# Kernel optimization log

Measured on AMD Instinct MI355X. Metric: run time of the kernel, lower is better.

The kernel has to match this reference:

```python
import jax, jax.numpy as jnp
import numpy as np

B = 16384
C = 2048  # in_channel
OUT = 2   # out_channel


def setup_inputs() -> dict:
    key = jax.random.key(0)
    k1, k2, k3, k4, k5, k6, k7 = jax.random.split(key, 7)
    scale = 1.0 / np.sqrt(3 * C)  # torch Linear default init range
    return {
        "s_f": jax.random.normal(k1, (B, C), dtype=jnp.float32),
        "g_f": jax.random.normal(k2, (B, C), dtype=jnp.float32),
        "v_f": jax.random.normal(k3, (B, C), dtype=jnp.float32),
        "W_aff": jax.random.uniform(k4, (3 * C, 3), dtype=jnp.float32, minval=-scale, maxval=scale),
        "b_aff": jax.random.uniform(k5, (3,), dtype=jnp.float32, minval=-scale, maxval=scale),
        "W_cls": jax.random.uniform(k6, (3 * C, OUT), dtype=jnp.float32, minval=-scale, maxval=scale),
        "b_cls": jax.random.uniform(k7, (OUT,), dtype=jnp.float32, minval=-scale, maxval=scale),
    }


def reference(s_f, g_f, v_f, W_aff, b_aff, W_cls, b_cls):
    # Attention gating over the three modalities.
    x_att = jnp.concatenate([s_f, g_f, v_f], axis=1)          # [B, 3C]
    att = jax.nn.softmax(x_att @ W_aff + b_aff, axis=1)       # [B, 3]
    # diag(att[:, i]) @ f  ==  per-row scalar scaling (broadcast multiply).
    s = att[:, 0:1] * s_f
    g = att[:, 1:2] * g_f
    v = att[:, 2:3] * v_f
    x = jnp.concatenate([s, g, v], axis=1)                    # [B, 3C]
    return jax.nn.softmax(x @ W_cls + b_cls, axis=1)          # [B, OUT]
```

## Files before the change

### kernel.cpp

```cpp
#include <hip/hip_runtime.h>

#define B_ROWS 16384
#define C_DIM  2048
#define BLK    512
#define CPT    4
#define RPB    32
#define RB     4
#define NITER  (RPB / RB)
#define GROUP  8
#define NWAVE  (BLK / 64)
#define NACC   5

#define DPP_ADD(v, ctrl, rmask) \
  v += __int_as_float(__builtin_amdgcn_update_dpp(0, __float_as_int(v), (ctrl), (rmask), 0xf, false))

__device__ __forceinline__ float wave_sum16(float v) {
  DPP_ADD(v, 0x111, 0xf);
  DPP_ADD(v, 0x112, 0xf);
  DPP_ADD(v, 0x114, 0xf);
  DPP_ADD(v, 0x118, 0xf);
  return v;
}

__global__ __launch_bounds__(BLK)
void maff_partial(const float* __restrict__ s_f,
                  const float* __restrict__ g_f,
                  const float* __restrict__ v_f,
                  const float* __restrict__ W_aff,
                  const float* __restrict__ W_cls,
                  float* __restrict__ ws)
{
  const int t    = threadIdx.x;
  const int lane = t & 63;
  const int wave = t >> 6;
  const int grp  = lane >> 4;
  const int m    = blockIdx.y;
  const int row0 = blockIdx.x * RPB;
  const int c0   = t * CPT;

  const float* f = (m == 0) ? s_f : (m == 1) ? g_f : v_f;

  float wa[CPT][3];
  float wc[CPT][2];
  {
    const float4* pa = (const float4*)(W_aff + ((size_t)m * C_DIM + c0) * 3);
    float4 a0 = pa[0], a1 = pa[1], a2 = pa[2];
    wa[0][0]=a0.x; wa[0][1]=a0.y; wa[0][2]=a0.z;
    wa[1][0]=a0.w; wa[1][1]=a1.x; wa[1][2]=a1.y;
    wa[2][0]=a1.z; wa[2][1]=a1.w; wa[2][2]=a2.x;
    wa[3][0]=a2.y; wa[3][1]=a2.z; wa[3][2]=a2.w;
    const float4* pc = (const float4*)(W_cls + ((size_t)m * C_DIM + c0) * 2);
    float4 q0 = pc[0], q1 = pc[1];
    wc[0][0]=q0.x; wc[0][1]=q0.y; wc[1][0]=q0.z; wc[1][1]=q0.w;
    wc[2][0]=q1.x; wc[2][1]=q1.y; wc[3][0]=q1.z; wc[3][1]=q1.w;
  }

  __shared__ float red[2][GROUP][NWAVE][4][NACC];

  const float* base = f + (size_t)row0 * C_DIM + c0;

  float4 cur[RB];
#pragma unroll
  for (int k = 0; k < RB; ++k)
    cur[k] = *(const float4*)(base + (size_t)k * C_DIM);

  for (int it = 0; it < NITER; ++it) {
    const int nit = (it + 1 < NITER) ? (it + 1) : it;
    float4 nxt[RB];
#pragma unroll
    for (int k = 0; k < RB; ++k)
      nxt[k] = *(const float4*)(base + (size_t)(nit * RB + k) * C_DIM);

    float acc[RB][NACC];
#pragma unroll
    for (int k = 0; k < RB; ++k) {
      float x[CPT] = {cur[k].x, cur[k].y, cur[k].z, cur[k].w};
      float p0 = 0.f, p1 = 0.f, p2 = 0.f, q0 = 0.f, q1 = 0.f;
#pragma unroll
      for (int i = 0; i < CPT; ++i) {
        p0 = fmaf(x[i], wa[i][0], p0);
        p1 = fmaf(x[i], wa[i][1], p1);
        p2 = fmaf(x[i], wa[i][2], p2);
        q0 = fmaf(x[i], wc[i][0], q0);
        q1 = fmaf(x[i], wc[i][1], q1);
      }
      acc[k][0] = p0; acc[k][1] = p1; acc[k][2] = p2;
      acc[k][3] = q0; acc[k][4] = q1;
    }

#pragma unroll
    for (int k = 0; k < RB; ++k)
#pragma unroll
      for (int j = 0; j < NACC; ++j)
        acc[k][j] = wave_sum16(acc[k][j]);

    const int g  = it >> 1;
    const int gb = g & 1;
#pragma unroll
    for (int k = 0; k < RB; ++k) {
      const int r  = it * RB + k;
      const int gs = r & (GROUP - 1);
      if ((lane & 15) == 15) {
        float* d = &red[gb][gs][wave][grp][0];
        d[0] = acc[k][0]; d[1] = acc[k][1]; d[2] = acc[k][2];
        d[3] = acc[k][3]; d[4] = acc[k][4];
      }
    }

    if (it & 1) {
      __syncthreads();
      if (t < GROUP) {
        float s[NACC] = {0.f, 0.f, 0.f, 0.f, 0.f};
        const float* z = &red[gb][t][0][0][0];
#pragma unroll
        for (int w = 0; w < NWAVE * 4; ++w)
#pragma unroll
          for (int j = 0; j < NACC; ++j)
            s[j] += z[w * NACC + j];
        const int row = row0 + g * GROUP + t;
#pragma unroll
        for (int j = 0; j < NACC; ++j)
          ws[(m * NACC + j) * B_ROWS + row] = s[j];
      }
    }

#pragma unroll
    for (int k = 0; k < RB; ++k) cur[k] = nxt[k];
  }
}

__global__ __launch_bounds__(256)
void maff_epilogue(const float* __restrict__ ws,
                   const float* __restrict__ b_aff,
                   const float* __restrict__ b_cls,
                   float* __restrict__ out)
{
  const int row = blockIdx.x * 256 + threadIdx.x;

  float P[3][NACC];
#pragma unroll
  for (int m = 0; m < 3; ++m)
#pragma unroll
    for (int j = 0; j < NACC; ++j)
      P[m][j] = ws[(m * NACC + j) * B_ROWS + row];

  float A0 = P[0][0] + P[1][0] + P[2][0] + b_aff[0];
  float A1 = P[0][1] + P[1][1] + P[2][1] + b_aff[1];
  float A2 = P[0][2] + P[1][2] + P[2][2] + b_aff[2];

  float mx = fmaxf(A0, fmaxf(A1, A2));
  float e0 = __expf(A0 - mx), e1 = __expf(A1 - mx), e2 = __expf(A2 - mx);
  float inv = 1.0f / (e0 + e1 + e2);
  float t0 = e0 * inv, t1 = e1 * inv, t2 = e2 * inv;

  float L0 = t0 * P[0][3] + t1 * P[1][3] + t2 * P[2][3] + b_cls[0];
  float L1 = t0 * P[0][4] + t1 * P[1][4] + t2 * P[2][4] + b_cls[1];
  float mm = fmaxf(L0, L1);
  float x0 = __expf(L0 - mm), x1 = __expf(L1 - mm);
  float is = 1.0f / (x0 + x1);

  *(float2*)(out + (size_t)row * 2) = make_float2(x0 * is, x1 * is);
}

extern "C" void kernel_launch(void* const* d_in, const int* in_sizes, int n_in,
                              void* d_out, int out_size, void* d_ws, size_t ws_size,
                              hipStream_t stream) {
  const float* s_f   = (const float*)d_in[0];
  const float* g_f   = (const float*)d_in[1];
  const float* v_f   = (const float*)d_in[2];
  const float* W_aff = (const float*)d_in[3];
  const float* b_aff = (const float*)d_in[4];
  const float* W_cls = (const float*)d_in[5];
  const float* b_cls = (const float*)d_in[6];
  float* out = (float*)d_out;
  float* ws  = (float*)d_ws;

  dim3 grid1(B_ROWS / RPB, 3);
  maff_partial<<<grid1, dim3(BLK), 0, stream>>>(s_f, g_f, v_f, W_aff, W_cls, ws);

  dim3 grid2(B_ROWS / 256);
  maff_epilogue<<<grid2, dim3(256), 0, stream>>>(ws, b_aff, b_cls, out);
}
```

Measured before the change: 362.0 us.

## Assign rows per wave with weights in LDS, eliminating block-level reductions

```diff
diff --git a/kernel.cpp b/kernel.cpp
--- a/kernel.cpp
+++ b/kernel.cpp
@@ -3,24 +3,14 @@
 #define B_ROWS 16384
 #define C_DIM  2048
 #define BLK    512
-#define CPT    4
-#define RPB    32
-#define RB     4
-#define NITER  (RPB / RB)
-#define GROUP  8
 #define NWAVE  (BLK / 64)
+#define RPW    4
+#define RPB    (NWAVE * RPW)
 #define NACC   5
+#define NCHUNK (C_DIM / 256)
 
 #define DPP_ADD(v, ctrl, rmask) \
   v += __int_as_float(__builtin_amdgcn_update_dpp(0, __float_as_int(v), (ctrl), (rmask), 0xf, false))
-
-__device__ __forceinline__ float wave_sum16(float v) {
-  DPP_ADD(v, 0x111, 0xf);
-  DPP_ADD(v, 0x112, 0xf);
-  DPP_ADD(v, 0x114, 0xf);
-  DPP_ADD(v, 0x118, 0xf);
-  return v;
-}
 
 __global__ __launch_bounds__(BLK)
 void maff_partial(const float* __restrict__ s_f,
@@ -33,99 +23,77 @@
   const int t    = threadIdx.x;
   const int lane = t & 63;
   const int wave = t >> 6;
-  const int grp  = lane >> 4;
   const int m    = blockIdx.y;
-  const int row0 = blockIdx.x * RPB;
-  const int c0   = t * CPT;
+  const int row0 = blockIdx.x * RPB + wave * RPW;
 
   const float* f = (m == 0) ? s_f : (m == 1) ? g_f : v_f;
 
-  float wa[CPT][3];
-  float wc[CPT][2];
+  __shared__ float4 W[NACC][BLK];
   {
-    const float4* pa = (const float4*)(W_aff + ((size_t)m * C_DIM + c0) * 3);
+    const float4* pa = (const float4*)(W_aff + ((size_t)m * C_DIM + t * 4) * 3);
     float4 a0 = pa[0], a1 = pa[1], a2 = pa[2];
-    wa[0][0]=a0.x; wa[0][1]=a0.y; wa[0][2]=a0.z;
-    wa[1][0]=a0.w; wa[1][1]=a1.x; wa[1][2]=a1.y;
-    wa[2][0]=a1.z; wa[2][1]=a1.w; wa[2][2]=a2.x;
-    wa[3][0]=a2.y; wa[3][1]=a2.z; wa[3][2]=a2.w;
-    const float4* pc = (const float4*)(W_cls + ((size_t)m * C_DIM + c0) * 2);
+    const float4* pc = (const float4*)(W_cls + ((size_t)m * C_DIM + t * 4) * 2);
     float4 q0 = pc[0], q1 = pc[1];
-    wc[0][0]=q0.x; wc[0][1]=q0.y; wc[1][0]=q0.z; wc[1][1]=q0.w;
-    wc[2][0]=q1.x; wc[2][1]=q1.y; wc[3][0]=q1.z; wc[3][1]=q1.w;
+    W[0][t] = make_float4(a0.x, a0.w, a1.z, a2.y);
+    W[1][t] = make_float4(a0.y, a1.x, a1.w, a2.z);
+    W[2][t] = make_float4(a0.z, a1.y, a2.x, a2.w);
+    W[3][t] = make_float4(q0.x, q0.z, q1.x, q1.z);
+    W[4][t] = make_float4(q0.y, q0.w, q1.y, q1.w);
+  }
+  __syncthreads();
+
+  const float4* wp = &W[0][lane];
+  const float*  fb = f + (size_t)row0 * C_DIM + lane * 4;
+
+  float acc[RPW][NACC];
+#pragma unroll
+  for (int r = 0; r < RPW; ++r)
+#pragma unroll
+    for (int j = 0; j < NACC; ++j)
+      acc[r][j] = 0.f;
+
+#pragma unroll
+  for (int ch = 0; ch < NCHUNK; ++ch) {
+    float4 x[RPW];
+#pragma unroll
+    for (int r = 0; r < RPW; ++r)
+      x[r] = *(const float4*)(fb + (size_t)r * C_DIM + ch * 256);
+
+    float4 wv[NACC];
+#pragma unroll
+    for (int j = 0; j < NACC; ++j)
+      wv[j] = wp[j * BLK + ch * 64];
+
+#pragma unroll
+    for (int r = 0; r < RPW; ++r)
+#pragma unroll
+      for (int j = 0; j < NACC; ++j)
+        acc[r][j] = fmaf(x[r].w, wv[j].w,
+                    fmaf(x[r].z, wv[j].z,
+                    fmaf(x[r].y, wv[j].y,
+                    fmaf(x[r].x, wv[j].x, acc[r][j]))));
   }
 
-  __shared__ float red[2][GROUP][NWAVE][4][NACC];
-
-  const float* base = f + (size_t)row0 * C_DIM + c0;
-
-  float4 cur[RB];
 #pragma unroll
-  for (int k = 0; k < RB; ++k)
-    cur[k] = *(const float4*)(base + (size_t)k * C_DIM);
-
-  for (int it = 0; it < NITER; ++it) {
-    const int nit = (it + 1 < NITER) ? (it + 1) : it;
-    float4 nxt[RB];
+  for (int r = 0; r < RPW; ++r)
 #pragma unroll
-    for (int k = 0; k < RB; ++k)
-      nxt[k] = *(const float4*)(base + (size_t)(nit * RB + k) * C_DIM);
-
-    float acc[RB][NACC];
-#pragma unroll
-    for (int k = 0; k < RB; ++k) {
-      float x[CPT] = {cur[k].x, cur[k].y, cur[k].z, cur[k].w};
-      float p0 = 0.f, p1 = 0.f, p2 = 0.f, q0 = 0.f, q1 = 0.f;
-#pragma unroll
-      for (int i = 0; i < CPT; ++i) {
-        p0 = fmaf(x[i], wa[i][0], p0);
-        p1 = fmaf(x[i], wa[i][1], p1);
-        p2 = fmaf(x[i], wa[i][2], p2);
-        q0 = fmaf(x[i], wc[i][0], q0);
-        q1 = fmaf(x[i], wc[i][1], q1);
-      }
-      acc[k][0] = p0; acc[k][1] = p1; acc[k][2] = p2;
-      acc[k][3] = q0; acc[k][4] = q1;
+    for (int j = 0; j < NACC; ++j) {
+      float v = acc[r][j];
+      DPP_ADD(v, 0x111, 0xf);
+      DPP_ADD(v, 0x112, 0xf);
+      DPP_ADD(v, 0x114, 0xf);
+      DPP_ADD(v, 0x118, 0xf);
+      DPP_ADD(v, 0x142, 0xa);
+      DPP_ADD(v, 0x143, 0xc);
+      acc[r][j] = v;
     }
 
+  if (lane == 63) {
 #pragma unroll
-    for (int k = 0; k < RB; ++k)
+    for (int r = 0; r < RPW; ++r)
 #pragma unroll
       for (int j = 0; j < NACC; ++j)
-        acc[k][j] = wave_sum16(acc[k][j]);
-
-    const int g  = it >> 1;
-    const int gb = g & 1;
-#pragma unroll
-    for (int k = 0; k < RB; ++k) {
-      const int r  = it * RB + k;
-      const int gs = r & (GROUP - 1);
-      if ((lane & 15) == 15) {
-        float* d = &red[gb][gs][wave][grp][0];
-        d[0] = acc[k][0]; d[1] = acc[k][1]; d[2] = acc[k][2];
-        d[3] = acc[k][3]; d[4] = acc[k][4];
-      }
-    }
-
-    if (it & 1) {
-      __syncthreads();
-      if (t < GROUP) {
-        float s[NACC] = {0.f, 0.f, 0.f, 0.f, 0.f};
-        const float* z = &red[gb][t][0][0][0];
-#pragma unroll
-        for (int w = 0; w < NWAVE * 4; ++w)
-#pragma unroll
-          for (int j = 0; j < NACC; ++j)
-            s[j] += z[w * NACC + j];
-        const int row = row0 + g * GROUP + t;
-#pragma unroll
-        for (int j = 0; j < NACC; ++j)
-          ws[(m * NACC + j) * B_ROWS + row] = s[j];
-      }
-    }
-
-#pragma unroll
-    for (int k = 0; k < RB; ++k) cur[k] = nxt[k];
+        ws[(size_t)(m * NACC + j) * B_ROWS + row0 + r] = acc[r][j];
   }
 }
 
```

After: 357.7 us. Within noise of the previous version (-1.2%).
